# Performance work log

Hardware: AMD Instinct MI355X
Metric: run time of the kernel (lower is better)

The kernel has to match this reference:

```python
import jax, jax.numpy as jnp
import numpy as np
from jax import lax

EPS = 1e-6
BLOCK_SIZE = 64


def _feature_map(x, W):
    # x: (B,H,N,S,D), W: (H,D,F) -> (B,H,N,S,2F), computed in fp32
    u = jnp.einsum('bhnsd,hdf->bhnsf', x, W).astype(jnp.float32)
    return jnp.concatenate([jax.nn.softmax(u, axis=-1), jax.nn.softmax(-u, axis=-1)], axis=-1)


def setup_inputs() -> dict:
    key = jax.random.key(0)
    k1, k2, k3, k4, k5 = jax.random.split(key, 5)
    B, H, L, D, F = 2, 16, 4096, 64, 64
    q = jax.random.normal(k1, (B, H, L, D), dtype=jnp.float32)
    k = jax.random.normal(k2, (B, H, L, D), dtype=jnp.float32)
    v = jax.random.normal(k3, (B, H, L, D), dtype=jnp.float32)
    # hedgehog_weights initialized as eye(D,F) per head, perturbed so the test is non-trivial
    W = jnp.eye(D, F, dtype=jnp.float32)[None].repeat(H, axis=0) + 0.02 * jax.random.normal(k4, (H, D, F), dtype=jnp.float32)
    alpha = 0.1 * jax.random.normal(k5, (1, H, 1, 1), dtype=jnp.float32)
    return {"query_states": q, "key_states": k, "value_states": v,
            "hedgehog_weights": W, "alpha": alpha}


def _forward(q, k, v, W, alpha):
    B, H, L, D = q.shape
    S = BLOCK_SIZE
    N = L // S  # L chosen divisible by block size (no padding path)
    scaling = D ** (-0.5)
    F2 = 2 * W.shape[-1]

    qb = q.reshape(B, H, N, S, D)
    kb = k.reshape(B, H, N, S, D)
    vb = v.reshape(B, H, N, S, D)
    phi_q = _feature_map(qb, W)  # (B,H,N,S,2F) fp32
    phi_k = _feature_map(kb, W)
    w = jax.nn.sigmoid(alpha)    # (1,H,1,1)

    def step(carry, xs):
        S_state, Z_state = carry            # (B,H,2F,D), (B,H,2F)
        qn, kn, vn, pqn, pkn = xs           # per-block slices
        # linear-attention branch (pre-update state = clean history)
        lin_num = jnp.einsum('bhsf,bhfd->bhsd', pqn, S_state)
        lin_den = jnp.maximum(jnp.einsum('bhsf,bhf->bhs', pqn, Z_state)[..., None], EPS)
        # intra-block softmax branch (unnormalized, shared denominator)
        scores = jnp.einsum('bhsd,bhtd->bhst', qn, kn) * scaling
        a = jnp.exp(scores - scores.max(axis=-1, keepdims=True))
        sm_num = jnp.einsum('bhst,bhtd->bhsd', a, vn)
        sm_den = jnp.maximum(a.sum(axis=-1, keepdims=True), EPS)
        out = (w * sm_num + lin_num) / jnp.maximum(w * sm_den + lin_den, EPS)
        # state update with this block's keys/values
        S_state = S_state + jnp.einsum('bhsf,bhsd->bhfd', pkn, vn)
        Z_state = Z_state + pkn.sum(axis=-2)
        return (S_state, Z_state), out

    init = (jnp.zeros((B, H, F2, D), jnp.float32), jnp.zeros((B, H, F2), jnp.float32))
    xs = (jnp.moveaxis(qb, 2, 0), jnp.moveaxis(kb, 2, 0), jnp.moveaxis(vb, 2, 0),
          jnp.moveaxis(phi_q, 2, 0), jnp.moveaxis(phi_k, 2, 0))
    _, outs = lax.scan(step, init, xs)       # (N,B,H,S,D)
    return jnp.moveaxis(outs, 0, 2).reshape(B, H, L, D)


def reference(query_states, key_states, value_states, hedgehog_weights, alpha):
    return _forward(query_states, key_states, value_states, hedgehog_weights, alpha)
```

## Files before the change

### kernel.cpp

```cpp
#include <hip/hip_runtime.h>
#include <hip/hip_bf16.h>
#include <math.h>

constexpr int Bc = 2, Hc = 16, Lc = 4096, Dc = 64, Fc = 64;
constexpr int Sc = 64;
constexpr int Nc = Lc / Sc;
constexpr int F2 = 2 * Fc;
constexpr int BH = Bc * Hc;
constexpr int NBLK = BH * Nc;
constexpr float EPSf = 1e-6f;
constexpr float SCALE = 0.125f;

typedef short short8 __attribute__((ext_vector_type(8)));
typedef float f32x4 __attribute__((ext_vector_type(4)));
typedef unsigned short ushort;
typedef ushort ushort4v __attribute__((ext_vector_type(4)));

__device__ inline ushort f2bf(float x) {
    unsigned u = __builtin_bit_cast(unsigned, x);
    u = (u + 0x7fffu + ((u >> 16) & 1u)) >> 16;
    return (ushort)u;
}
__device__ inline float bf2f(ushort h) {
    return __builtin_bit_cast(float, ((unsigned)h) << 16);
}
__device__ inline f32x4 zero4() { f32x4 z = {0.f, 0.f, 0.f, 0.f}; return z; }

__device__ inline f32x4 mfma(short8 a, short8 b, f32x4 c) {
    return __builtin_amdgcn_mfma_f32_16x16x32_bf16(a, b, c, 0, 0, 0);
}

__device__ inline short8 ldfrag(const char* L, int row, int chunk, int rowbytes, int mask) {
    return *(const short8*)(L + row * rowbytes + ((chunk * 16) ^ ((row & mask) << 4)));
}

__device__ inline void stage_rm(const float* __restrict__ src, char* dst, int t) {
    #pragma unroll
    for (int i = 0; i < 4; ++i) {
        int e = t + i * 256;
        float4 x = ((const float4*)src)[e];
        int r = e >> 4;
        int c4 = (e & 15) * 4;
        ushort4v hv;
        hv[0] = f2bf(x.x); hv[1] = f2bf(x.y); hv[2] = f2bf(x.z); hv[3] = f2bf(x.w);
        *(ushort4v*)(dst + r * 128 + ((c4 * 2) ^ ((r & 7) << 4))) = hv;
    }
}

__device__ inline void stage_tr(const float* __restrict__ src, char* dst, int t) {
    int j = t & 63, g = t >> 6;
    #pragma unroll
    for (int i = 0; i < 4; ++i) {
        int i0 = g * 4 + i * 16;
        ushort4v hv;
        #pragma unroll
        for (int jj = 0; jj < 4; ++jj) hv[jj] = f2bf(src[(i0 + jj) * 64 + j]);
        *(ushort4v*)(dst + j * 128 + ((2 * i0) ^ ((j & 7) << 4))) = hv;
    }
}

__global__ __launch_bounds__(256) void passA(const float* __restrict__ K,
                                             const float* __restrict__ V,
                                             const float* __restrict__ W,
                                             ushort* __restrict__ wsS,
                                             float* __restrict__ wsZ)
{
    __shared__ __align__(16) char lds[40960];
    char* kR = lds;
    char* WT = lds + 8192;
    char* vT = lds + 16384;
    char* pT = lds + 24576;

    const int t = threadIdx.x, wv = t >> 6, l = t & 63, lr = l & 15, lg = l >> 4;
    const int bid = blockIdx.x, bh = bid >> 6, h = bh & (Hc - 1);
    const long base = (long)bh * Lc * Dc + (long)(bid & 63) * Sc * Dc;

    stage_rm(K + base, kR, t);
    stage_tr(W + (long)h * Dc * Fc, WT, t);
    stage_tr(V + base, vT, t);
    __syncthreads();

    short8 af0 = ldfrag(kR, 16 * wv + lr, lg, 128, 7);
    short8 af1 = ldfrag(kR, 16 * wv + lr, 4 + lg, 128, 7);
    f32x4 u0[4];
    #pragma unroll
    for (int tf = 0; tf < 4; ++tf) u0[tf] = zero4();
    #pragma unroll
    for (int tf = 0; tf < 4; ++tf) {
        u0[tf] = mfma(af0, ldfrag(WT, tf * 16 + lr, lg, 128, 7), u0[tf]);
        u0[tf] = mfma(af1, ldfrag(WT, tf * 16 + lr, 4 + lg, 128, 7), u0[tf]);
    }

    float pp[4][4], pn[4][4];
    #pragma unroll
    for (int r = 0; r < 4; ++r) {
        float mx = fmaxf(fmaxf(u0[0][r], u0[1][r]), fmaxf(u0[2][r], u0[3][r]));
        float mn = fminf(fminf(u0[0][r], u0[1][r]), fminf(u0[2][r], u0[3][r]));
        #pragma unroll
        for (int m = 1; m < 16; m <<= 1) {
            mx = fmaxf(mx, __shfl_xor(mx, m, 16));
            mn = fminf(mn, __shfl_xor(mn, m, 16));
        }
        float sp = 0.f, sn = 0.f;
        #pragma unroll
        for (int tf = 0; tf < 4; ++tf) {
            pp[tf][r] = __expf(u0[tf][r] - mx); sp += pp[tf][r];
            pn[tf][r] = __expf(mn - u0[tf][r]); sn += pn[tf][r];
        }
        #pragma unroll
        for (int m = 1; m < 16; m <<= 1) {
            sp += __shfl_xor(sp, m, 16);
            sn += __shfl_xor(sn, m, 16);
        }
        float rp = 1.f / sp, rn = 1.f / sn;
        #pragma unroll
        for (int tf = 0; tf < 4; ++tf) { pp[tf][r] *= rp; pn[tf][r] *= rn; }
    }

    #pragma unroll
    for (int tf = 0; tf < 4; ++tf)
        #pragma unroll
        for (int r = 0; r < 4; ++r) {
            int s = 16 * wv + lg * 4 + r;
            int f = tf * 16 + lr;
            *(ushort*)(pT + f * 128 + ((2 * s) ^ ((f & 7) << 4))) = f2bf(pp[tf][r]);
            int fn = 64 + f;
            *(ushort*)(pT + fn * 128 + ((2 * s) ^ ((fn & 7) << 4))) = f2bf(pn[tf][r]);
        }
    __syncthreads();

    short8 av0 = ldfrag(vT, 16 * wv + lr, lg, 128, 7);
    short8 av1 = ldfrag(vT, 16 * wv + lr, 4 + lg, 128, 7);
    f32x4 acc[8];
    #pragma unroll
    for (int tf = 0; tf < 8; ++tf) acc[tf] = zero4();
    #pragma unroll
    for (int tf = 0; tf < 8; ++tf) {
        acc[tf] = mfma(av0, ldfrag(pT, tf * 16 + lr, lg, 128, 7), acc[tf]);
        acc[tf] = mfma(av1, ldfrag(pT, tf * 16 + lr, 4 + lg, 128, 7), acc[tf]);
    }
    ushort* o = wsS + (long)bid * (F2 * Dc);
    #pragma unroll
    for (int tf = 0; tf < 8; ++tf)
        #pragma unroll
        for (int r = 0; r < 4; ++r) {
            int d = 16 * wv + lg * 4 + r;
            o[d * 128 + tf * 16 + lr] = f2bf(acc[tf][r]);
        }

    if (t < 128) {
        float z = 0.f;
        #pragma unroll
        for (int c = 0; c < 8; ++c) {
            short8 vv = ldfrag(pT, t, c, 128, 7);
            #pragma unroll
            for (int j = 0; j < 8; ++j) z += bf2f((ushort)vv[j]);
        }
        wsZ[(long)bid * F2 + t] = z;
    }
}

__global__ __launch_bounds__(256) void passB(ushort* __restrict__ wsS,
                                             float* __restrict__ wsZ)
{
    const int t = threadIdx.x;
    const int bh = blockIdx.x >> 3, chunk = blockIdx.x & 7;
    const int eoff = chunk * 1024 + t * 4;
    float c0 = 0.f, c1 = 0.f, c2 = 0.f, c3 = 0.f, zc = 0.f;
    const bool doZ = (chunk == 0) && (t < F2);
    for (int n = 0; n < Nc; ++n) {
        ushort4v* p = (ushort4v*)(wsS + (long)(bh * Nc + n) * 8192 + eoff);
        ushort4v x = *p;
        ushort4v cc;
        cc[0] = f2bf(c0); cc[1] = f2bf(c1); cc[2] = f2bf(c2); cc[3] = f2bf(c3);
        *p = cc;
        c0 += bf2f(x[0]); c1 += bf2f(x[1]); c2 += bf2f(x[2]); c3 += bf2f(x[3]);
        if (doZ) {
            float* pz = wsZ + (long)(bh * Nc + n) * F2 + t;
            float zv = *pz; *pz = zc; zc += zv;
        }
    }
}

__global__ __launch_bounds__(256) void passC(const float* __restrict__ Q,
                                             const float* __restrict__ K,
                                             const float* __restrict__ V,
                                             const float* __restrict__ W,
                                             const float* __restrict__ Alpha,
                                             const ushort* __restrict__ wsS,
                                             const float* __restrict__ wsZ,
                                             float* __restrict__ Out)
{
    __shared__ __align__(16) char lds[49664];
    char* qR   = lds;
    char* WT   = lds + 8192;
    char* kR   = lds + 16384;
    char* phiB = lds;
    char* aB   = lds + 16384;
    char* vT   = lds + 24576;
    char* St   = lds + 32768;
    float* sZ  = (float*)(lds + 49152);

    const int t = threadIdx.x, wv = t >> 6, l = t & 63, lr = l & 15, lg = l >> 4;
    const int bid = blockIdx.x, bh = bid >> 6, h = bh & (Hc - 1);
    const long base = (long)bh * Lc * Dc + (long)(bid & 63) * Sc * Dc;

    stage_rm(Q + base, qR, t);
    stage_tr(W + (long)h * Dc * Fc, WT, t);
    stage_rm(K + base, kR, t);
    stage_tr(V + base, vT, t);
    {
        const ushort* g = wsS + (long)bid * (F2 * Dc);
        #pragma unroll
        for (int i = 0; i < 4; ++i) {
            int c = t + i * 256;
            int d = c >> 4, fc = c & 15;
            short8 x = ((const short8*)g)[c];
            *(short8*)(St + d * 256 + ((fc * 16) ^ ((d & 15) << 4))) = x;
        }
        if (t < F2) sZ[t] = wsZ[(long)bid * F2 + t];
    }
    __syncthreads();

    short8 aq0 = ldfrag(qR, 16 * wv + lr, lg, 128, 7);
    short8 aq1 = ldfrag(qR, 16 * wv + lr, 4 + lg, 128, 7);
    f32x4 u0[4], s0[4];
    #pragma unroll
    for (int tf = 0; tf < 4; ++tf) { u0[tf] = zero4(); s0[tf] = zero4(); }
    #pragma unroll
    for (int tf = 0; tf < 4; ++tf) {
        u0[tf] = mfma(aq0, ldfrag(WT, tf * 16 + lr, lg, 128, 7), u0[tf]);
        u0[tf] = mfma(aq1, ldfrag(WT, tf * 16 + lr, 4 + lg, 128, 7), u0[tf]);
        s0[tf] = mfma(aq0, ldfrag(kR, tf * 16 + lr, lg, 128, 7), s0[tf]);
        s0[tf] = mfma(aq1, ldfrag(kR, tf * 16 + lr, 4 + lg, 128, 7), s0[tf]);
    }

    float pp[4][4], pn[4][4], sden[4], lden[4];
    #pragma unroll
    for (int r = 0; r < 4; ++r) {
        float mx = fmaxf(fmaxf(u0[0][r], u0[1][r]), fmaxf(u0[2][r], u0[3][r]));
        float mn = fminf(fminf(u0[0][r], u0[1][r]), fminf(u0[2][r], u0[3][r]));
        #pragma unroll
        for (int m = 1; m < 16; m <<= 1) {
            mx = fmaxf(mx, __shfl_xor(mx, m, 16));
            mn = fminf(mn, __shfl_xor(mn, m, 16));
        }
        float sp = 0.f, sn = 0.f;
        #pragma unroll
        for (int tf = 0; tf < 4; ++tf) {
            pp[tf][r] = __expf(u0[tf][r] - mx); sp += pp[tf][r];
            pn[tf][r] = __expf(mn - u0[tf][r]); sn += pn[tf][r];
        }
        #pragma unroll
        for (int m = 1; m < 16; m <<= 1) {
            sp += __shfl_xor(sp, m, 16);
            sn += __shfl_xor(sn, m, 16);
        }
        float rp = 1.f / sp, rn = 1.f / sn;
        float zd = 0.f;
        #pragma unroll
        for (int tf = 0; tf < 4; ++tf) {
            pp[tf][r] *= rp; pn[tf][r] *= rn;
            zd += pp[tf][r] * sZ[tf * 16 + lr] + pn[tf][r] * sZ[64 + tf * 16 + lr];
        }
        #pragma unroll
        for (int m = 1; m < 16; m <<= 1) zd += __shfl_xor(zd, m, 16);
        lden[r] = fmaxf(zd, EPSf);

        float sc[4];
        #pragma unroll
        for (int tf = 0; tf < 4; ++tf) sc[tf] = s0[tf][r] * SCALE;
        float m2 = fmaxf(fmaxf(sc[0], sc[1]), fmaxf(sc[2], sc[3]));
        #pragma unroll
        for (int m = 1; m < 16; m <<= 1) m2 = fmaxf(m2, __shfl_xor(m2, m, 16));
        float as = 0.f;
        #pragma unroll
        for (int tf = 0; tf < 4; ++tf) { sc[tf] = __expf(sc[tf] - m2); as += sc[tf]; }
        #pragma unroll
        for (int m = 1; m < 16; m <<= 1) as += __shfl_xor(as, m, 16);
        sden[r] = fmaxf(as, EPSf);
        #pragma unroll
        for (int tf = 0; tf < 4; ++tf) s0[tf][r] = sc[tf];
    }
    __syncthreads();

    #pragma unroll
    for (int tf = 0; tf < 4; ++tf)
        #pragma unroll
        for (int r = 0; r < 4; ++r) {
            int s = 16 * wv + lg * 4 + r;
            int f = tf * 16 + lr;
            *(ushort*)(phiB + s * 256 + ((2 * f) ^ ((s & 15) << 4))) = f2bf(pp[tf][r]);
            *(ushort*)(phiB + s * 256 + ((2 * (64 + f)) ^ ((s & 15) << 4))) = f2bf(pn[tf][r]);
            *(ushort*)(aB + s * 128 + ((2 * f) ^ ((s & 7) << 4))) = f2bf(s0[tf][r]);
        }
    __syncthreads();

    f32x4 acc[4];
    #pragma unroll
    for (int td = 0; td < 4; ++td) acc[td] = zero4();
    short8 aa0 = ldfrag(aB, 16 * wv + lr, lg, 128, 7);
    short8 aa1 = ldfrag(aB, 16 * wv + lr, 4 + lg, 128, 7);
    #pragma unroll
    for (int td = 0; td < 4; ++td) {
        acc[td] = mfma(aa0, ldfrag(vT, td * 16 + lr, lg, 128, 7), acc[td]);
        acc[td] = mfma(aa1, ldfrag(vT, td * 16 + lr, 4 + lg, 128, 7), acc[td]);
    }
    const float w = 1.f / (1.f + __expf(-Alpha[h]));
    #pragma unroll
    for (int td = 0; td < 4; ++td)
        #pragma unroll
        for (int r = 0; r < 4; ++r) acc[td][r] *= w;

    short8 pf[4];
    #pragma unroll
    for (int kc = 0; kc < 4; ++kc) pf[kc] = ldfrag(phiB, 16 * wv + lr, kc * 4 + lg, 256, 15);
    #pragma unroll
    for (int td = 0; td < 4; ++td)
        #pragma unroll
        for (int kc = 0; kc < 4; ++kc)
            acc[td] = mfma(pf[kc], ldfrag(St, td * 16 + lr, kc * 4 + lg, 256, 15), acc[td]);

    float* op = Out + base;
    #pragma unroll
    for (int r = 0; r < 4; ++r) {
        int s = 16 * wv + lg * 4 + r;
        float den = fmaxf(w * sden[r] + lden[r], EPSf);
        float inv = 1.f / den;
        #pragma unroll
        for (int td = 0; td < 4; ++td)
            op[s * 64 + td * 16 + lr] = acc[td][r] * inv;
    }
}

extern "C" void kernel_launch(void* const* d_in, const int* in_sizes, int n_in,
                              void* d_out, int out_size, void* d_ws, size_t ws_size,
                              hipStream_t stream)
{
    const float* q     = (const float*)d_in[0];
    const float* k     = (const float*)d_in[1];
    const float* v     = (const float*)d_in[2];
    const float* W     = (const float*)d_in[3];
    const float* alpha = (const float*)d_in[4];
    float* out = (float*)d_out;

    ushort* wsSb = (ushort*)d_ws;
    float*  wsZ  = (float*)((char*)d_ws + (size_t)NBLK * F2 * Dc * 2);

    passA<<<NBLK, 256, 0, stream>>>(k, v, W, wsSb, wsZ);
    passB<<<256, 256, 0, stream>>>(wsSb, wsZ);
    passC<<<NBLK, 256, 0, stream>>>(q, k, v, W, alpha, wsSb, wsZ, out);
}
```

Baseline: 86.84 us.

## Load MFMA fragments directly from global memory and batch scan loads

Adds a pre-pass that transposes W to bf16 once per head. passA and passC now read K, Q, W and the prefix state S directly from global memory into MFMA fragments instead of staging them in LDS, which shrinks LDS use and drops a barrier. passB issues 32 loads at a time per chunk before its serial prefix scan and moves the Z scan into separate blocks. The cost is more uncoalesced, redundant global reads: each K row is converted to bf16 several times in passC, and one extra kernel launch is added.

```diff
diff --git a/kernel.cpp b/kernel.cpp
--- a/kernel.cpp
+++ b/kernel.cpp
@@ -34,17 +34,16 @@
     return *(const short8*)(L + row * rowbytes + ((chunk * 16) ^ ((row & mask) << 4)));
 }
 
-__device__ inline void stage_rm(const float* __restrict__ src, char* dst, int t) {
-    #pragma unroll
-    for (int i = 0; i < 4; ++i) {
-        int e = t + i * 256;
-        float4 x = ((const float4*)src)[e];
-        int r = e >> 4;
-        int c4 = (e & 15) * 4;
-        ushort4v hv;
-        hv[0] = f2bf(x.x); hv[1] = f2bf(x.y); hv[2] = f2bf(x.z); hv[3] = f2bf(x.w);
-        *(ushort4v*)(dst + r * 128 + ((c4 * 2) ^ ((r & 7) << 4))) = hv;
-    }
+__device__ inline short8 gfrag_f32(const float* __restrict__ base, int row, int chunk) {
+    const float4* p = (const float4*)(base + row * 64 + chunk * 8);
+    float4 a = p[0], b = p[1];
+    short8 r;
+    r[0] = (short)f2bf(a.x); r[1] = (short)f2bf(a.y); r[2] = (short)f2bf(a.z); r[3] = (short)f2bf(a.w);
+    r[4] = (short)f2bf(b.x); r[5] = (short)f2bf(b.y); r[6] = (short)f2bf(b.z); r[7] = (short)f2bf(b.w);
+    return r;
+}
+__device__ inline short8 gfrag_bf16(const ushort* __restrict__ base, int row, int chunk, int rowlen) {
+    return *(const short8*)(base + row * rowlen + chunk * 8);
 }
 
 __device__ inline void stage_tr(const float* __restrict__ src, char* dst, int t) {
@@ -59,36 +58,48 @@
     }
 }
 
+__global__ __launch_bounds__(256) void passW(const float* __restrict__ W,
+                                             ushort* __restrict__ Wt)
+{
+    const int h = blockIdx.x, t = threadIdx.x;
+    const int f = t & 63, g = t >> 6;
+    const float* src = W + (long)h * 4096;
+    ushort* dst = Wt + (long)h * 4096;
+    #pragma unroll
+    for (int i = 0; i < 16; ++i) {
+        int d = g * 16 + i;
+        dst[f * 64 + d] = f2bf(src[d * 64 + f]);
+    }
+}
+
 __global__ __launch_bounds__(256) void passA(const float* __restrict__ K,
                                              const float* __restrict__ V,
-                                             const float* __restrict__ W,
+                                             const ushort* __restrict__ Wt,
                                              ushort* __restrict__ wsS,
                                              float* __restrict__ wsZ)
 {
-    __shared__ __align__(16) char lds[40960];
-    char* kR = lds;
-    char* WT = lds + 8192;
-    char* vT = lds + 16384;
-    char* pT = lds + 24576;
+    __shared__ __align__(16) char lds[24576];
+    char* vT = lds;
+    char* pT = lds + 8192;
 
     const int t = threadIdx.x, wv = t >> 6, l = t & 63, lr = l & 15, lg = l >> 4;
     const int bid = blockIdx.x, bh = bid >> 6, h = bh & (Hc - 1);
-    const long base = (long)bh * Lc * Dc + (long)(bid & 63) * Sc * Dc;
-
-    stage_rm(K + base, kR, t);
-    stage_tr(W + (long)h * Dc * Fc, WT, t);
+    const long base = (long)bh * (Lc * Dc) + (long)(bid & 63) * (Sc * Dc);
+
     stage_tr(V + base, vT, t);
-    __syncthreads();
-
-    short8 af0 = ldfrag(kR, 16 * wv + lr, lg, 128, 7);
-    short8 af1 = ldfrag(kR, 16 * wv + lr, 4 + lg, 128, 7);
+
+    const float* kp = K + base;
+    const ushort* wt = Wt + (long)h * 4096;
+
+    short8 ak0 = gfrag_f32(kp, 16 * wv + lr, lg);
+    short8 ak1 = gfrag_f32(kp, 16 * wv + lr, 4 + lg);
     f32x4 u0[4];
     #pragma unroll
     for (int tf = 0; tf < 4; ++tf) u0[tf] = zero4();
     #pragma unroll
     for (int tf = 0; tf < 4; ++tf) {
-        u0[tf] = mfma(af0, ldfrag(WT, tf * 16 + lr, lg, 128, 7), u0[tf]);
-        u0[tf] = mfma(af1, ldfrag(WT, tf * 16 + lr, 4 + lg, 128, 7), u0[tf]);
+        u0[tf] = mfma(ak0, gfrag_bf16(wt, tf * 16 + lr, lg, 64), u0[tf]);
+        u0[tf] = mfma(ak1, gfrag_bf16(wt, tf * 16 + lr, 4 + lg, 64), u0[tf]);
     }
 
     float pp[4][4], pn[4][4];
@@ -164,20 +175,37 @@
                                              float* __restrict__ wsZ)
 {
     const int t = threadIdx.x;
+    if (blockIdx.x >= 256) {
+        const int bh = blockIdx.x - 256;
+        if (t < 128) {
+            float zc = 0.f, zb[32];
+            #pragma unroll
+            for (int h2 = 0; h2 < 2; ++h2) {
+                float* zp = wsZ + ((long)bh * 64 + h2 * 32) * 128 + t;
+                #pragma unroll
+                for (int i = 0; i < 32; ++i) zb[i] = zp[i * 128];
+                #pragma unroll
+                for (int i = 0; i < 32; ++i) { float x = zb[i]; zp[i * 128] = zc; zc += x; }
+            }
+        }
+        return;
+    }
     const int bh = blockIdx.x >> 3, chunk = blockIdx.x & 7;
-    const int eoff = chunk * 1024 + t * 4;
-    float c0 = 0.f, c1 = 0.f, c2 = 0.f, c3 = 0.f, zc = 0.f;
-    const bool doZ = (chunk == 0) && (t < F2);
-    for (int n = 0; n < Nc; ++n) {
-        ushort4v* p = (ushort4v*)(wsS + (long)(bh * Nc + n) * 8192 + eoff);
-        ushort4v x = *p;
-        ushort4v cc;
-        cc[0] = f2bf(c0); cc[1] = f2bf(c1); cc[2] = f2bf(c2); cc[3] = f2bf(c3);
-        *p = cc;
-        c0 += bf2f(x[0]); c1 += bf2f(x[1]); c2 += bf2f(x[2]); c3 += bf2f(x[3]);
-        if (doZ) {
-            float* pz = wsZ + (long)(bh * Nc + n) * F2 + t;
-            float zv = *pz; *pz = zc; zc += zv;
+    ushort* p = wsS + (long)bh * 64 * 8192 + chunk * 1024 + t * 4;
+    float c0 = 0.f, c1 = 0.f, c2 = 0.f, c3 = 0.f;
+    ushort4v buf[32];
+    #pragma unroll
+    for (int h2 = 0; h2 < 2; ++h2) {
+        ushort4v* pp = (ushort4v*)(p + (long)h2 * 32 * 8192);
+        #pragma unroll
+        for (int i = 0; i < 32; ++i) buf[i] = pp[i * 2048];
+        #pragma unroll
+        for (int i = 0; i < 32; ++i) {
+            ushort4v x = buf[i];
+            ushort4v cc;
+            cc[0] = f2bf(c0); cc[1] = f2bf(c1); cc[2] = f2bf(c2); cc[3] = f2bf(c3);
+            pp[i * 2048] = cc;
+            c0 += bf2f(x[0]); c1 += bf2f(x[1]); c2 += bf2f(x[2]); c3 += bf2f(x[3]);
         }
     }
 }
@@ -185,54 +213,44 @@
 __global__ __launch_bounds__(256) void passC(const float* __restrict__ Q,
                                              const float* __restrict__ K,
                                              const float* __restrict__ V,
-                                             const float* __restrict__ W,
+                                             const ushort* __restrict__ Wt,
                                              const float* __restrict__ Alpha,
                                              const ushort* __restrict__ wsS,
                                              const float* __restrict__ wsZ,
                                              float* __restrict__ Out)
 {
-    __shared__ __align__(16) char lds[49664];
-    char* qR   = lds;
-    char* WT   = lds + 8192;
-    char* kR   = lds + 16384;
-    char* phiB = lds;
-    char* aB   = lds + 16384;
-    char* vT   = lds + 24576;
-    char* St   = lds + 32768;
-    float* sZ  = (float*)(lds + 49152);
-
+    __shared__ __align__(16) char lds[32768];
+    char* vT = lds;
     const int t = threadIdx.x, wv = t >> 6, l = t & 63, lr = l & 15, lg = l >> 4;
+    char* phiL = lds + 8192 + wv * 4096;
+    char* aL   = lds + 24576 + wv * 2048;
+
     const int bid = blockIdx.x, bh = bid >> 6, h = bh & (Hc - 1);
-    const long base = (long)bh * Lc * Dc + (long)(bid & 63) * Sc * Dc;
-
-    stage_rm(Q + base, qR, t);
-    stage_tr(W + (long)h * Dc * Fc, WT, t);
-    stage_rm(K + base, kR, t);
+    const long base = (long)bh * (Lc * Dc) + (long)(bid & 63) * (Sc * Dc);
+
     stage_tr(V + base, vT, t);
-    {
-        const ushort* g = wsS + (long)bid * (F2 * Dc);
-        #pragma unroll
-        for (int i = 0; i < 4; ++i) {
-            int c = t + i * 256;
-            int d = c >> 4, fc = c & 15;
-            short8 x = ((const short8*)g)[c];
-            *(short8*)(St + d * 256 + ((fc * 16) ^ ((d & 15) << 4))) = x;
-        }
-        if (t < F2) sZ[t] = wsZ[(long)bid * F2 + t];
-    }
-    __syncthreads();
-
-    short8 aq0 = ldfrag(qR, 16 * wv + lr, lg, 128, 7);
-    short8 aq1 = ldfrag(qR, 16 * wv + lr, 4 + lg, 128, 7);
+
+    const float* qp = Q + base;
+    const float* kp = K + base;
+    const ushort* wt = Wt + (long)h * 4096;
+    const float* zp = wsZ + (long)bid * F2;
+
+    float zv[4], zn[4];
+    #pragma unroll
+    for (int tf = 0; tf < 4; ++tf) { zv[tf] = zp[tf * 16 + lr]; zn[tf] = zp[64 + tf * 16 + lr]; }
+    const float w = 1.f / (1.f + __expf(-Alpha[h]));
+
+    short8 aq0 = gfrag_f32(qp, 16 * wv + lr, lg);
+    short8 aq1 = gfrag_f32(qp, 16 * wv + lr, 4 + lg);
     f32x4 u0[4], s0[4];
     #pragma unroll
     for (int tf = 0; tf < 4; ++tf) { u0[tf] = zero4(); s0[tf] = zero4(); }
     #pragma unroll
     for (int tf = 0; tf < 4; ++tf) {
-        u0[tf] = mfma(aq0, ldfrag(WT, tf * 16 + lr, lg, 128, 7), u0[tf]);
-        u0[tf] = mfma(aq1, ldfrag(WT, tf * 16 + lr, 4 + lg, 128, 7), u0[tf]);
-        s0[tf] = mfma(aq0, ldfrag(kR, tf * 16 + lr, lg, 128, 7), s0[tf]);
-        s0[tf] = mfma(aq1, ldfrag(kR, tf * 16 + lr, 4 + lg, 128, 7), s0[tf]);
+        u0[tf] = mfma(aq0, gfrag_bf16(wt, tf * 16 + lr, lg, 64), u0[tf]);
+        u0[tf] = mfma(aq1, gfrag_bf16(wt, tf * 16 + lr, 4 + lg, 64), u0[tf]);
+        s0[tf] = mfma(aq0, gfrag_f32(kp, tf * 16 + lr, lg), s0[tf]);
+        s0[tf] = mfma(aq1, gfrag_f32(kp, tf * 16 + lr, 4 + lg), s0[tf]);
     }
 
     float pp[4][4], pn[4][4], sden[4], lden[4];
@@ -261,7 +279,7 @@
         #pragma unroll
         for (int tf = 0; tf < 4; ++tf) {
             pp[tf][r] *= rp; pn[tf][r] *= rn;
-            zd += pp[tf][r] * sZ[tf * 16 + lr] + pn[tf][r] * sZ[64 + tf * 16 + lr];
+            zd += pp[tf][r] * zv[tf] + pn[tf][r] * zn[tf];
         }
         #pragma unroll
         for (int m = 1; m < 16; m <<= 1) zd += __shfl_xor(zd, m, 16);
@@ -282,31 +300,31 @@
         #pragma unroll
         for (int tf = 0; tf < 4; ++tf) s0[tf][r] = sc[tf];
     }
+
+    #pragma unroll
+    for (int tf = 0; tf < 4; ++tf)
+        #pragma unroll
+        for (int r = 0; r < 4; ++r) {
+            int sl = lg * 4 + r;
+            int f = tf * 16 + lr;
+            *(ushort*)(phiL + sl * 256 + ((2 * f) ^ ((sl & 15) << 4))) = f2bf(pp[tf][r]);
+            *(ushort*)(phiL + sl * 256 + ((2 * (64 + f)) ^ ((sl & 15) << 4))) = f2bf(pn[tf][r]);
+            *(ushort*)(aL + sl * 128 + ((2 * f) ^ ((sl & 7) << 4))) = f2bf(s0[tf][r]);
+        }
+
     __syncthreads();
 
-    #pragma unroll
-    for (int tf = 0; tf < 4; ++tf)
-        #pragma unroll
-        for (int r = 0; r < 4; ++r) {
-            int s = 16 * wv + lg * 4 + r;
-            int f = tf * 16 + lr;
-            *(ushort*)(phiB + s * 256 + ((2 * f) ^ ((s & 15) << 4))) = f2bf(pp[tf][r]);
-            *(ushort*)(phiB + s * 256 + ((2 * (64 + f)) ^ ((s & 15) << 4))) = f2bf(pn[tf][r]);
-            *(ushort*)(aB + s * 128 + ((2 * f) ^ ((s & 7) << 4))) = f2bf(s0[tf][r]);
-        }
-    __syncthreads();
-
+    const ushort* Sg = wsS + (long)bid * (F2 * Dc);
     f32x4 acc[4];
     #pragma unroll
     for (int td = 0; td < 4; ++td) acc[td] = zero4();
-    short8 aa0 = ldfrag(aB, 16 * wv + lr, lg, 128, 7);
-    short8 aa1 = ldfrag(aB, 16 * wv + lr, 4 + lg, 128, 7);
+    short8 aa0 = ldfrag(aL, lr, lg, 128, 7);
+    short8 aa1 = ldfrag(aL, lr, 4 + lg, 128, 7);
     #pragma unroll
     for (int td = 0; td < 4; ++td) {
         acc[td] = mfma(aa0, ldfrag(vT, td * 16 + lr, lg, 128, 7), acc[td]);
         acc[td] = mfma(aa1, ldfrag(vT, td * 16 + lr, 4 + lg, 128, 7), acc[td]);
     }
-    const float w = 1.f / (1.f + __expf(-Alpha[h]));
     #pragma unroll
     for (int td = 0; td < 4; ++td)
         #pragma unroll
@@ -314,12 +332,12 @@
 
     short8 pf[4];
     #pragma unroll
-    for (int kc = 0; kc < 4; ++kc) pf[kc] = ldfrag(phiB, 16 * wv + lr, kc * 4 + lg, 256, 15);
+    for (int kc = 0; kc < 4; ++kc) pf[kc] = ldfrag(phiL, lr, kc * 4 + lg, 256, 15);
     #pragma unroll
     for (int td = 0; td < 4; ++td)
         #pragma unroll
         for (int kc = 0; kc < 4; ++kc)
-            acc[td] = mfma(pf[kc], ldfrag(St, td * 16 + lr, kc * 4 + lg, 256, 15), acc[td]);
+            acc[td] = mfma(pf[kc], gfrag_bf16(Sg, td * 16 + lr, kc * 4 + lg, 128), acc[td]);
 
     float* op = Out + base;
     #pragma unroll
@@ -346,8 +364,10 @@
 
     ushort* wsSb = (ushort*)d_ws;
     float*  wsZ  = (float*)((char*)d_ws + (size_t)NBLK * F2 * Dc * 2);
-
-    passA<<<NBLK, 256, 0, stream>>>(k, v, W, wsSb, wsZ);
-    passB<<<256, 256, 0, stream>>>(wsSb, wsZ);
-    passC<<<NBLK, 256, 0, stream>>>(q, k, v, W, alpha, wsSb, wsZ, out);
-}
+    ushort* Wtb  = (ushort*)((char*)wsZ + (size_t)NBLK * F2 * 4);
+
+    passW<<<Hc, 256, 0, stream>>>(W, Wtb);
+    passA<<<NBLK, 256, 0, stream>>>(k, v, Wtb, wsSb, wsZ);
+    passB<<<288, 256, 0, stream>>>(wsSb, wsZ);
+    passC<<<NBLK, 256, 0, stream>>>(q, k, v, Wtb, alpha, wsSb, wsZ, out);
+}
```

After: 94.75 us. 9.1% more time.

## Process chunks of four blocks per workgroup with in-register running state

Applied to the files above, without the earlier changes.

Each workgroup now handles a chunk of four 64-row blocks instead of one. The first pass accumulates the chunk's key-value state in fp32, the scan pass works over 16 chunks per head instead of 64 blocks, and the final pass carries the state in registers while it updates block by block. This shrinks the workspace traffic and the length of the serial scan, and it drops the bf16 rounding of prefix states. In exchange the final pass runs a sequential four-step loop per workgroup with fewer workgroups (512), uses more LDS (about 74 KB), and drops the max-subtraction in the feature-map softmax, which could overflow for large inputs.

```diff
diff --git a/kernel.cpp b/kernel.cpp
--- a/kernel.cpp
+++ b/kernel.cpp
@@ -2,12 +2,13 @@
 #include <hip/hip_bf16.h>
 #include <math.h>
 
-constexpr int Bc = 2, Hc = 16, Lc = 4096, Dc = 64, Fc = 64;
-constexpr int Sc = 64;
+constexpr int Hc = 16, Lc = 4096, Dc = 64, Sc = 64;
 constexpr int Nc = Lc / Sc;
-constexpr int F2 = 2 * Fc;
-constexpr int BH = Bc * Hc;
-constexpr int NBLK = BH * Nc;
+constexpr int F2 = 128;
+constexpr int BH = 32;
+constexpr int CH = 4;
+constexpr int CPB = Nc / CH;
+constexpr int NCHUNK = BH * CPB;
 constexpr float EPSf = 1e-6f;
 constexpr float SCALE = 0.125f;
 
@@ -21,9 +22,6 @@
     u = (u + 0x7fffu + ((u >> 16) & 1u)) >> 16;
     return (ushort)u;
 }
-__device__ inline float bf2f(ushort h) {
-    return __builtin_bit_cast(float, ((unsigned)h) << 16);
-}
 __device__ inline f32x4 zero4() { f32x4 z = {0.f, 0.f, 0.f, 0.f}; return z; }
 
 __device__ inline f32x4 mfma(short8 a, short8 b, f32x4 c) {
@@ -32,6 +30,15 @@
 
 __device__ inline short8 ldfrag(const char* L, int row, int chunk, int rowbytes, int mask) {
     return *(const short8*)(L + row * rowbytes + ((chunk * 16) ^ ((row & mask) << 4)));
+}
+
+__device__ inline short8 gfrag_f32(const float* __restrict__ base, int row, int chunk) {
+    const float4* p = (const float4*)(base + row * 64 + chunk * 8);
+    float4 a = p[0], b = p[1];
+    short8 r;
+    r[0] = (short)f2bf(a.x); r[1] = (short)f2bf(a.y); r[2] = (short)f2bf(a.z); r[3] = (short)f2bf(a.w);
+    r[4] = (short)f2bf(b.x); r[5] = (short)f2bf(b.y); r[6] = (short)f2bf(b.z); r[7] = (short)f2bf(b.w);
+    return r;
 }
 
 __device__ inline void stage_rm(const float* __restrict__ src, char* dst, int t) {
@@ -59,277 +66,360 @@
     }
 }
 
-__global__ __launch_bounds__(256) void passA(const float* __restrict__ K,
-                                             const float* __restrict__ V,
-                                             const float* __restrict__ W,
-                                             ushort* __restrict__ wsS,
-                                             float* __restrict__ wsZ)
+__global__ __launch_bounds__(256) void passF1(const float* __restrict__ K,
+                                              const float* __restrict__ V,
+                                              const float* __restrict__ W,
+                                              float* __restrict__ wsC,
+                                              float* __restrict__ wsZc)
 {
-    __shared__ __align__(16) char lds[40960];
-    char* kR = lds;
-    char* WT = lds + 8192;
-    char* vT = lds + 16384;
-    char* pT = lds + 24576;
+    __shared__ __align__(16) char lds[51200];
+    char* kR  = lds;
+    char* vT0 = lds + 8192;
+    char* vT1 = lds + 16384;
+    char* WTl = lds + 24576;
+    char* pT  = lds + 32768;
+    float* Zp = (float*)(lds + 49152);
 
     const int t = threadIdx.x, wv = t >> 6, l = t & 63, lr = l & 15, lg = l >> 4;
-    const int bid = blockIdx.x, bh = bid >> 6, h = bh & (Hc - 1);
-    const long base = (long)bh * Lc * Dc + (long)(bid & 63) * Sc * Dc;
-
-    stage_rm(K + base, kR, t);
-    stage_tr(W + (long)h * Dc * Fc, WT, t);
-    stage_tr(V + base, vT, t);
+    const int bid = blockIdx.x, bh = bid >> 4, c = bid & (CPB - 1), h = bh & (Hc - 1);
+    const long hbase = (long)bh * (Lc * Dc);
+
+    stage_tr(W + (long)h * (Dc * 64), WTl, t);
+
+    f32x4 acc[8];
+    #pragma unroll
+    for (int i = 0; i < 8; ++i) acc[i] = zero4();
+    float zpa[4] = {0.f,0.f,0.f,0.f}, zna[4] = {0.f,0.f,0.f,0.f};
+
+    for (int tt = 0; tt < CH; ++tt) {
+        char* vT = (tt & 1) ? vT1 : vT0;
+        const long base = hbase + (long)(c * CH + tt) * (Sc * Dc);
+        stage_rm(K + base, kR, t);
+        stage_tr(V + base, vT, t);
+        __syncthreads();
+
+        short8 ak0 = ldfrag(kR, 16*wv + lr, lg, 128, 7);
+        short8 ak1 = ldfrag(kR, 16*wv + lr, 4 + lg, 128, 7);
+        f32x4 u0[4];
+        #pragma unroll
+        for (int tf = 0; tf < 4; ++tf) u0[tf] = zero4();
+        #pragma unroll
+        for (int tf = 0; tf < 4; ++tf) {
+            u0[tf] = mfma(ak0, ldfrag(WTl, tf*16 + lr, lg, 128, 7), u0[tf]);
+            u0[tf] = mfma(ak1, ldfrag(WTl, tf*16 + lr, 4 + lg, 128, 7), u0[tf]);
+        }
+        float pp[4][4], pn[4][4];
+        #pragma unroll
+        for (int r = 0; r < 4; ++r) {
+            float sp = 0.f, sn = 0.f;
+            #pragma unroll
+            for (int tf = 0; tf < 4; ++tf) {
+                pp[tf][r] = __expf(u0[tf][r]);  sp += pp[tf][r];
+                pn[tf][r] = __expf(-u0[tf][r]); sn += pn[tf][r];
+            }
+            #pragma unroll
+            for (int m = 1; m < 16; m <<= 1) { sp += __shfl_xor(sp, m, 16); sn += __shfl_xor(sn, m, 16); }
+            float rp = 1.f / sp, rn = 1.f / sn;
+            #pragma unroll
+            for (int tf = 0; tf < 4; ++tf) {
+                pp[tf][r] *= rp; pn[tf][r] *= rn;
+                zpa[tf] += pp[tf][r]; zna[tf] += pn[tf][r];
+            }
+        }
+        #pragma unroll
+        for (int tf = 0; tf < 4; ++tf)
+            #pragma unroll
+            for (int r = 0; r < 4; ++r) {
+                int s = 16*wv + lg*4 + r;
+                int f = tf*16 + lr;
+                *(ushort*)(pT + f*128 + ((2*s) ^ ((f & 7) << 4))) = f2bf(pp[tf][r]);
+                int fn = 64 + f;
+                *(ushort*)(pT + fn*128 + ((2*s) ^ ((fn & 7) << 4))) = f2bf(pn[tf][r]);
+            }
+        __syncthreads();
+
+        short8 av0 = ldfrag(vT, 16*wv + lr, lg, 128, 7);
+        short8 av1 = ldfrag(vT, 16*wv + lr, 4 + lg, 128, 7);
+        #pragma unroll
+        for (int tf = 0; tf < 8; ++tf) {
+            acc[tf] = mfma(av0, ldfrag(pT, tf*16 + lr, lg, 128, 7), acc[tf]);
+            acc[tf] = mfma(av1, ldfrag(pT, tf*16 + lr, 4 + lg, 128, 7), acc[tf]);
+        }
+    }
+
+    float* oc = wsC + (long)bid * 8192;
+    #pragma unroll
+    for (int tf = 0; tf < 8; ++tf)
+        #pragma unroll
+        for (int r = 0; r < 4; ++r)
+            oc[(16*wv + lg*4 + r) * 128 + tf*16 + lr] = acc[tf][r];
+
+    #pragma unroll
+    for (int tf = 0; tf < 4; ++tf) {
+        zpa[tf] += __shfl_xor(zpa[tf], 16); zpa[tf] += __shfl_xor(zpa[tf], 32);
+        zna[tf] += __shfl_xor(zna[tf], 16); zna[tf] += __shfl_xor(zna[tf], 32);
+    }
+    if (l < 16) {
+        #pragma unroll
+        for (int tf = 0; tf < 4; ++tf) {
+            Zp[wv*128 + tf*16 + lr]      = zpa[tf];
+            Zp[wv*128 + 64 + tf*16 + lr] = zna[tf];
+        }
+    }
     __syncthreads();
-
-    short8 af0 = ldfrag(kR, 16 * wv + lr, lg, 128, 7);
-    short8 af1 = ldfrag(kR, 16 * wv + lr, 4 + lg, 128, 7);
-    f32x4 u0[4];
-    #pragma unroll
-    for (int tf = 0; tf < 4; ++tf) u0[tf] = zero4();
-    #pragma unroll
-    for (int tf = 0; tf < 4; ++tf) {
-        u0[tf] = mfma(af0, ldfrag(WT, tf * 16 + lr, lg, 128, 7), u0[tf]);
-        u0[tf] = mfma(af1, ldfrag(WT, tf * 16 + lr, 4 + lg, 128, 7), u0[tf]);
-    }
-
-    float pp[4][4], pn[4][4];
-    #pragma unroll
-    for (int r = 0; r < 4; ++r) {
-        float mx = fmaxf(fmaxf(u0[0][r], u0[1][r]), fmaxf(u0[2][r], u0[3][r]));
-        float mn = fminf(fminf(u0[0][r], u0[1][r]), fminf(u0[2][r], u0[3][r]));
-        #pragma unroll
-        for (int m = 1; m < 16; m <<= 1) {
-            mx = fmaxf(mx, __shfl_xor(mx, m, 16));
-            mn = fminf(mn, __shfl_xor(mn, m, 16));
-        }
-        float sp = 0.f, sn = 0.f;
-        #pragma unroll
-        for (int tf = 0; tf < 4; ++tf) {
-            pp[tf][r] = __expf(u0[tf][r] - mx); sp += pp[tf][r];
-            pn[tf][r] = __expf(mn - u0[tf][r]); sn += pn[tf][r];
-        }
-        #pragma unroll
-        for (int m = 1; m < 16; m <<= 1) {
-            sp += __shfl_xor(sp, m, 16);
-            sn += __shfl_xor(sn, m, 16);
-        }
-        float rp = 1.f / sp, rn = 1.f / sn;
-        #pragma unroll
-        for (int tf = 0; tf < 4; ++tf) { pp[tf][r] *= rp; pn[tf][r] *= rn; }
-    }
-
-    #pragma unroll
-    for (int tf = 0; tf < 4; ++tf)
-        #pragma unroll
-        for (int r = 0; r < 4; ++r) {
-            int s = 16 * wv + lg * 4 + r;
-            int f = tf * 16 + lr;
-            *(ushort*)(pT + f * 128 + ((2 * s) ^ ((f & 7) << 4))) = f2bf(pp[tf][r]);
-            int fn = 64 + f;
-            *(ushort*)(pT + fn * 128 + ((2 * s) ^ ((fn & 7) << 4))) = f2bf(pn[tf][r]);
-        }
-    __syncthreads();
-
-    short8 av0 = ldfrag(vT, 16 * wv + lr, lg, 128, 7);
-    short8 av1 = ldfrag(vT, 16 * wv + lr, 4 + lg, 128, 7);
-    f32x4 acc[8];
-    #pragma unroll
-    for (int tf = 0; tf < 8; ++tf) acc[tf] = zero4();
-    #pragma unroll
-    for (int tf = 0; tf < 8; ++tf) {
-        acc[tf] = mfma(av0, ldfrag(pT, tf * 16 + lr, lg, 128, 7), acc[tf]);
-        acc[tf] = mfma(av1, ldfrag(pT, tf * 16 + lr, 4 + lg, 128, 7), acc[tf]);
-    }
-    ushort* o = wsS + (long)bid * (F2 * Dc);
-    #pragma unroll
-    for (int tf = 0; tf < 8; ++tf)
-        #pragma unroll
-        for (int r = 0; r < 4; ++r) {
-            int d = 16 * wv + lg * 4 + r;
-            o[d * 128 + tf * 16 + lr] = f2bf(acc[tf][r]);
-        }
-
-    if (t < 128) {
-        float z = 0.f;
-        #pragma unroll
-        for (int c = 0; c < 8; ++c) {
-            short8 vv = ldfrag(pT, t, c, 128, 7);
-            #pragma unroll
-            for (int j = 0; j < 8; ++j) z += bf2f((ushort)vv[j]);
-        }
-        wsZ[(long)bid * F2 + t] = z;
-    }
-}
-
-__global__ __launch_bounds__(256) void passB(ushort* __restrict__ wsS,
-                                             float* __restrict__ wsZ)
+    if (t < 128)
+        wsZc[(long)bid * 128 + t] = Zp[t] + Zp[128 + t] + Zp[256 + t] + Zp[384 + t];
+}
+
+__global__ __launch_bounds__(256) void passF2(float* __restrict__ wsC,
+                                              float* __restrict__ wsZc)
 {
     const int t = threadIdx.x;
-    const int bh = blockIdx.x >> 3, chunk = blockIdx.x & 7;
-    const int eoff = chunk * 1024 + t * 4;
-    float c0 = 0.f, c1 = 0.f, c2 = 0.f, c3 = 0.f, zc = 0.f;
-    const bool doZ = (chunk == 0) && (t < F2);
-    for (int n = 0; n < Nc; ++n) {
-        ushort4v* p = (ushort4v*)(wsS + (long)(bh * Nc + n) * 8192 + eoff);
-        ushort4v x = *p;
-        ushort4v cc;
-        cc[0] = f2bf(c0); cc[1] = f2bf(c1); cc[2] = f2bf(c2); cc[3] = f2bf(c3);
-        *p = cc;
-        c0 += bf2f(x[0]); c1 += bf2f(x[1]); c2 += bf2f(x[2]); c3 += bf2f(x[3]);
-        if (doZ) {
-            float* pz = wsZ + (long)(bh * Nc + n) * F2 + t;
-            float zv = *pz; *pz = zc; zc += zv;
-        }
-    }
-}
-
-__global__ __launch_bounds__(256) void passC(const float* __restrict__ Q,
-                                             const float* __restrict__ K,
-                                             const float* __restrict__ V,
-                                             const float* __restrict__ W,
-                                             const float* __restrict__ Alpha,
-                                             const ushort* __restrict__ wsS,
-                                             const float* __restrict__ wsZ,
-                                             float* __restrict__ Out)
+    if (blockIdx.x >= 256) {
+        const int bh = blockIdx.x - 256;
+        if (t < 128) {
+            float* zp = wsZc + (long)bh * CPB * 128 + t;
+            float buf[CPB];
+            #pragma unroll
+            for (int i = 0; i < CPB; ++i) buf[i] = zp[(long)i * 128];
+            float cz = 0.f;
+            #pragma unroll
+            for (int i = 0; i < CPB; ++i) { float x = buf[i]; zp[(long)i * 128] = cz; cz += x; }
+        }
+        return;
+    }
+    const int bh = blockIdx.x >> 3, part = blockIdx.x & 7;
+    float* p = wsC + (long)bh * CPB * 8192 + part * 1024 + t * 4;
+    float4 buf[CPB];
+    #pragma unroll
+    for (int i = 0; i < CPB; ++i) buf[i] = *(const float4*)(p + (long)i * 8192);
+    float4 cr = make_float4(0.f, 0.f, 0.f, 0.f);
+    #pragma unroll
+    for (int i = 0; i < CPB; ++i) {
+        float4 x = buf[i];
+        *(float4*)(p + (long)i * 8192) = cr;
+        cr.x += x.x; cr.y += x.y; cr.z += x.z; cr.w += x.w;
+    }
+}
+
+__global__ __launch_bounds__(256) void passF3(const float* __restrict__ Q,
+                                              const float* __restrict__ K,
+                                              const float* __restrict__ V,
+                                              const float* __restrict__ W,
+                                              const float* __restrict__ Alpha,
+                                              const float* __restrict__ wsC,
+                                              const float* __restrict__ wsZc,
+                                              float* __restrict__ Out)
 {
-    __shared__ __align__(16) char lds[49664];
-    char* qR   = lds;
-    char* WT   = lds + 8192;
-    char* kR   = lds + 16384;
-    char* phiB = lds;
-    char* aB   = lds + 16384;
-    char* vT   = lds + 24576;
-    char* St   = lds + 32768;
-    float* sZ  = (float*)(lds + 49152);
+    __shared__ __align__(16) char lds[75776];
+    char* kR   = lds;
+    char* vT0  = lds + 8192;
+    char* vT1  = lds + 16384;
+    char* WTl  = lds + 24576;
+    char* Stb  = lds + 32768;
+    char* phiP = lds + 49152;
+    char* aLb  = lds + 65536;
+    float* Zp  = (float*)(lds + 73728);
 
     const int t = threadIdx.x, wv = t >> 6, l = t & 63, lr = l & 15, lg = l >> 4;
-    const int bid = blockIdx.x, bh = bid >> 6, h = bh & (Hc - 1);
-    const long base = (long)bh * Lc * Dc + (long)(bid & 63) * Sc * Dc;
-
-    stage_rm(Q + base, qR, t);
-    stage_tr(W + (long)h * Dc * Fc, WT, t);
-    stage_rm(K + base, kR, t);
-    stage_tr(V + base, vT, t);
+    char* phiL = phiP + wv * 4096;
+    char* aL   = aLb + wv * 2048;
+    char* pT   = phiP;
+
+    const int bid = blockIdx.x, bh = bid >> 4, c = bid & (CPB - 1), h = bh & (Hc - 1);
+    const long hbase = (long)bh * (Lc * Dc);
+
+    stage_tr(W + (long)h * (Dc * 64), WTl, t);
+
+    f32x4 sacc[8];
     {
-        const ushort* g = wsS + (long)bid * (F2 * Dc);
-        #pragma unroll
-        for (int i = 0; i < 4; ++i) {
-            int c = t + i * 256;
-            int d = c >> 4, fc = c & 15;
-            short8 x = ((const short8*)g)[c];
-            *(short8*)(St + d * 256 + ((fc * 16) ^ ((d & 15) << 4))) = x;
-        }
-        if (t < F2) sZ[t] = wsZ[(long)bid * F2 + t];
-    }
-    __syncthreads();
-
-    short8 aq0 = ldfrag(qR, 16 * wv + lr, lg, 128, 7);
-    short8 aq1 = ldfrag(qR, 16 * wv + lr, 4 + lg, 128, 7);
-    f32x4 u0[4], s0[4];
-    #pragma unroll
-    for (int tf = 0; tf < 4; ++tf) { u0[tf] = zero4(); s0[tf] = zero4(); }
-    #pragma unroll
-    for (int tf = 0; tf < 4; ++tf) {
-        u0[tf] = mfma(aq0, ldfrag(WT, tf * 16 + lr, lg, 128, 7), u0[tf]);
-        u0[tf] = mfma(aq1, ldfrag(WT, tf * 16 + lr, 4 + lg, 128, 7), u0[tf]);
-        s0[tf] = mfma(aq0, ldfrag(kR, tf * 16 + lr, lg, 128, 7), s0[tf]);
-        s0[tf] = mfma(aq1, ldfrag(kR, tf * 16 + lr, 4 + lg, 128, 7), s0[tf]);
-    }
-
-    float pp[4][4], pn[4][4], sden[4], lden[4];
-    #pragma unroll
-    for (int r = 0; r < 4; ++r) {
-        float mx = fmaxf(fmaxf(u0[0][r], u0[1][r]), fmaxf(u0[2][r], u0[3][r]));
-        float mn = fminf(fminf(u0[0][r], u0[1][r]), fminf(u0[2][r], u0[3][r]));
-        #pragma unroll
-        for (int m = 1; m < 16; m <<= 1) {
-            mx = fmaxf(mx, __shfl_xor(mx, m, 16));
-            mn = fminf(mn, __shfl_xor(mn, m, 16));
-        }
-        float sp = 0.f, sn = 0.f;
+        const float* s0p = wsC + (long)bid * 8192;
+        #pragma unroll
+        for (int tf = 0; tf < 8; ++tf)
+            #pragma unroll
+            for (int r = 0; r < 4; ++r)
+                sacc[tf][r] = s0p[(16*wv + lg*4 + r) * 128 + tf*16 + lr];
+    }
+    float zv[4], zn_[4];
+    {
+        const float* z0 = wsZc + (long)bid * 128;
+        #pragma unroll
+        for (int tf = 0; tf < 4; ++tf) { zv[tf] = z0[tf*16 + lr]; zn_[tf] = z0[64 + tf*16 + lr]; }
+    }
+    const float w = 1.f / (1.f + __expf(-Alpha[h]));
+
+    for (int tt = 0; tt < CH; ++tt) {
+        char* vT = (tt & 1) ? vT1 : vT0;
+        const long base = hbase + (long)(c * CH + tt) * (Sc * Dc);
+
+        #pragma unroll
+        for (int tf = 0; tf < 8; ++tf)
+            #pragma unroll
+            for (int r = 0; r < 4; ++r) {
+                int d = 16*wv + lg*4 + r;
+                int f = tf*16 + lr;
+                *(ushort*)(Stb + d*256 + ((2*f) ^ ((d & 15) << 4))) = f2bf(sacc[tf][r]);
+            }
+        stage_rm(K + base, kR, t);
+        stage_tr(V + base, vT, t);
+        short8 aq0 = gfrag_f32(Q + base, 16*wv + lr, lg);
+        short8 aq1 = gfrag_f32(Q + base, 16*wv + lr, 4 + lg);
+        __syncthreads();
+
+        short8 ak0 = ldfrag(kR, 16*wv + lr, lg, 128, 7);
+        short8 ak1 = ldfrag(kR, 16*wv + lr, 4 + lg, 128, 7);
+        f32x4 uq[4], uk[4], sc0[4];
+        #pragma unroll
+        for (int tf = 0; tf < 4; ++tf) { uq[tf] = zero4(); uk[tf] = zero4(); sc0[tf] = zero4(); }
+        const bool upd = (tt != CH - 1);
         #pragma unroll
         for (int tf = 0; tf < 4; ++tf) {
-            pp[tf][r] = __expf(u0[tf][r] - mx); sp += pp[tf][r];
-            pn[tf][r] = __expf(mn - u0[tf][r]); sn += pn[tf][r];
-        }
-        #pragma unroll
-        for (int m = 1; m < 16; m <<= 1) {
-            sp += __shfl_xor(sp, m, 16);
-            sn += __shfl_xor(sn, m, 16);
-        }
-        float rp = 1.f / sp, rn = 1.f / sn;
-        float zd = 0.f;
-        #pragma unroll
-        for (int tf = 0; tf < 4; ++tf) {
-            pp[tf][r] *= rp; pn[tf][r] *= rn;
-            zd += pp[tf][r] * sZ[tf * 16 + lr] + pn[tf][r] * sZ[64 + tf * 16 + lr];
-        }
-        #pragma unroll
-        for (int m = 1; m < 16; m <<= 1) zd += __shfl_xor(zd, m, 16);
-        lden[r] = fmaxf(zd, EPSf);
-
-        float sc[4];
-        #pragma unroll
-        for (int tf = 0; tf < 4; ++tf) sc[tf] = s0[tf][r] * SCALE;
-        float m2 = fmaxf(fmaxf(sc[0], sc[1]), fmaxf(sc[2], sc[3]));
-        #pragma unroll
-        for (int m = 1; m < 16; m <<= 1) m2 = fmaxf(m2, __shfl_xor(m2, m, 16));
-        float as = 0.f;
-        #pragma unroll
-        for (int tf = 0; tf < 4; ++tf) { sc[tf] = __expf(sc[tf] - m2); as += sc[tf]; }
-        #pragma unroll
-        for (int m = 1; m < 16; m <<= 1) as += __shfl_xor(as, m, 16);
-        sden[r] = fmaxf(as, EPSf);
-        #pragma unroll
-        for (int tf = 0; tf < 4; ++tf) s0[tf][r] = sc[tf];
-    }
-    __syncthreads();
-
-    #pragma unroll
-    for (int tf = 0; tf < 4; ++tf)
+            short8 bw0 = ldfrag(WTl, tf*16 + lr, lg, 128, 7);
+            short8 bw1 = ldfrag(WTl, tf*16 + lr, 4 + lg, 128, 7);
+            uq[tf] = mfma(aq0, bw0, uq[tf]); uq[tf] = mfma(aq1, bw1, uq[tf]);
+            sc0[tf] = mfma(aq0, ldfrag(kR, tf*16 + lr, lg, 128, 7), sc0[tf]);
+            sc0[tf] = mfma(aq1, ldfrag(kR, tf*16 + lr, 4 + lg, 128, 7), sc0[tf]);
+            if (upd) { uk[tf] = mfma(ak0, bw0, uk[tf]); uk[tf] = mfma(ak1, bw1, uk[tf]); }
+        }
+
+        float lden[4], sden[4];
         #pragma unroll
         for (int r = 0; r < 4; ++r) {
-            int s = 16 * wv + lg * 4 + r;
-            int f = tf * 16 + lr;
-            *(ushort*)(phiB + s * 256 + ((2 * f) ^ ((s & 15) << 4))) = f2bf(pp[tf][r]);
-            *(ushort*)(phiB + s * 256 + ((2 * (64 + f)) ^ ((s & 15) << 4))) = f2bf(pn[tf][r]);
-            *(ushort*)(aB + s * 128 + ((2 * f) ^ ((s & 7) << 4))) = f2bf(s0[tf][r]);
-        }
-    __syncthreads();
-
-    f32x4 acc[4];
-    #pragma unroll
-    for (int td = 0; td < 4; ++td) acc[td] = zero4();
-    short8 aa0 = ldfrag(aB, 16 * wv + lr, lg, 128, 7);
-    short8 aa1 = ldfrag(aB, 16 * wv + lr, 4 + lg, 128, 7);
-    #pragma unroll
-    for (int td = 0; td < 4; ++td) {
-        acc[td] = mfma(aa0, ldfrag(vT, td * 16 + lr, lg, 128, 7), acc[td]);
-        acc[td] = mfma(aa1, ldfrag(vT, td * 16 + lr, 4 + lg, 128, 7), acc[td]);
-    }
-    const float w = 1.f / (1.f + __expf(-Alpha[h]));
-    #pragma unroll
-    for (int td = 0; td < 4; ++td)
-        #pragma unroll
-        for (int r = 0; r < 4; ++r) acc[td][r] *= w;
-
-    short8 pf[4];
-    #pragma unroll
-    for (int kc = 0; kc < 4; ++kc) pf[kc] = ldfrag(phiB, 16 * wv + lr, kc * 4 + lg, 256, 15);
-    #pragma unroll
-    for (int td = 0; td < 4; ++td)
-        #pragma unroll
-        for (int kc = 0; kc < 4; ++kc)
-            acc[td] = mfma(pf[kc], ldfrag(St, td * 16 + lr, kc * 4 + lg, 256, 15), acc[td]);
-
-    float* op = Out + base;
-    #pragma unroll
-    for (int r = 0; r < 4; ++r) {
-        int s = 16 * wv + lg * 4 + r;
-        float den = fmaxf(w * sden[r] + lden[r], EPSf);
-        float inv = 1.f / den;
+            float pqp[4], pqn[4];
+            float sp = 0.f, sn = 0.f;
+            #pragma unroll
+            for (int tf = 0; tf < 4; ++tf) {
+                pqp[tf] = __expf(uq[tf][r]);  sp += pqp[tf];
+                pqn[tf] = __expf(-uq[tf][r]); sn += pqn[tf];
+            }
+            #pragma unroll
+            for (int m = 1; m < 16; m <<= 1) { sp += __shfl_xor(sp, m, 16); sn += __shfl_xor(sn, m, 16); }
+            float rp = 1.f / sp, rn = 1.f / sn;
+            float zd = 0.f;
+            #pragma unroll
+            for (int tf = 0; tf < 4; ++tf) {
+                pqp[tf] *= rp; pqn[tf] *= rn;
+                zd += pqp[tf] * zv[tf] + pqn[tf] * zn_[tf];
+            }
+            #pragma unroll
+            for (int m = 1; m < 16; m <<= 1) zd += __shfl_xor(zd, m, 16);
+            lden[r] = fmaxf(zd, EPSf);
+            int sl = lg*4 + r;
+            #pragma unroll
+            for (int tf = 0; tf < 4; ++tf) {
+                int f = tf*16 + lr;
+                *(ushort*)(phiL + sl*256 + ((2*f) ^ ((sl & 15) << 4))) = f2bf(pqp[tf]);
+                *(ushort*)(phiL + sl*256 + ((2*(64 + f)) ^ ((sl & 15) << 4))) = f2bf(pqn[tf]);
+            }
+        }
+
+        #pragma unroll
+        for (int r = 0; r < 4; ++r) {
+            float s[4];
+            #pragma unroll
+            for (int tf = 0; tf < 4; ++tf) s[tf] = sc0[tf][r] * SCALE;
+            float m2 = fmaxf(fmaxf(s[0], s[1]), fmaxf(s[2], s[3]));
+            #pragma unroll
+            for (int m = 1; m < 16; m <<= 1) m2 = fmaxf(m2, __shfl_xor(m2, m, 16));
+            float as = 0.f;
+            #pragma unroll
+            for (int tf = 0; tf < 4; ++tf) { s[tf] = __expf(s[tf] - m2); as += s[tf]; }
+            #pragma unroll
+            for (int m = 1; m < 16; m <<= 1) as += __shfl_xor(as, m, 16);
+            sden[r] = fmaxf(as, EPSf);
+            int sl = lg*4 + r;
+            #pragma unroll
+            for (int tf = 0; tf < 4; ++tf)
+                *(ushort*)(aL + sl*128 + ((2*(tf*16 + lr)) ^ ((sl & 7) << 4))) = f2bf(w * s[tf]);
+        }
+
+        f32x4 oacc[4];
+        #pragma unroll
+        for (int td = 0; td < 4; ++td) oacc[td] = zero4();
+        short8 aa0 = ldfrag(aL, lr, lg, 128, 7);
+        short8 aa1 = ldfrag(aL, lr, 4 + lg, 128, 7);
+        #pragma unroll
+        for (int td = 0; td < 4; ++td) {
+            oacc[td] = mfma(aa0, ldfrag(vT, td*16 + lr, lg, 128, 7), oacc[td]);
+            oacc[td] = mfma(aa1, ldfrag(vT, td*16 + lr, 4 + lg, 128, 7), oacc[td]);
+        }
+        short8 pf[4];
+        #pragma unroll
+        for (int kc = 0; kc < 4; ++kc) pf[kc] = ldfrag(phiL, lr, kc*4 + lg, 256, 15);
         #pragma unroll
         for (int td = 0; td < 4; ++td)
-            op[s * 64 + td * 16 + lr] = acc[td][r] * inv;
+            #pragma unroll
+            for (int kc = 0; kc < 4; ++kc)
+                oacc[td] = mfma(pf[kc], ldfrag(Stb, td*16 + lr, kc*4 + lg, 256, 15), oacc[td]);
+
+        float* op = Out + base;
+        #pragma unroll
+        for (int r = 0; r < 4; ++r) {
+            int s = 16*wv + lg*4 + r;
+            float inv = 1.f / fmaxf(w * sden[r] + lden[r], EPSf);
+            #pragma unroll
+            for (int td = 0; td < 4; ++td)
+                op[s*64 + td*16 + lr] = oacc[td][r] * inv;
+        }
+
+        if (upd) {
+            __syncthreads();
+            float pkp[4][4], pkn[4][4];
+            float zr[4] = {0.f,0.f,0.f,0.f}, zrn[4] = {0.f,0.f,0.f,0.f};
+            #pragma unroll
+            for (int r = 0; r < 4; ++r) {
+                float sp = 0.f, sn = 0.f;
+                #pragma unroll
+                for (int tf = 0; tf < 4; ++tf) {
+                    pkp[tf][r] = __expf(uk[tf][r]);  sp += pkp[tf][r];
+                    pkn[tf][r] = __expf(-uk[tf][r]); sn += pkn[tf][r];
+                }
+                #pragma unroll
+                for (int m = 1; m < 16; m <<= 1) { sp += __shfl_xor(sp, m, 16); sn += __shfl_xor(sn, m, 16); }
+                float rp = 1.f / sp, rn = 1.f / sn;
+                #pragma unroll
+                for (int tf = 0; tf < 4; ++tf) {
+                    pkp[tf][r] *= rp; pkn[tf][r] *= rn;
+                    zr[tf] += pkp[tf][r]; zrn[tf] += pkn[tf][r];
+                }
+            }
+            #pragma unroll
+            for (int tf = 0; tf < 4; ++tf)
+                #pragma unroll
+                for (int r = 0; r < 4; ++r) {
+                    int s = 16*wv + lg*4 + r;
+                    int f = tf*16 + lr;
+                    *(ushort*)(pT + f*128 + ((2*s) ^ ((f & 7) << 4))) = f2bf(pkp[tf][r]);
+                    int fn = 64 + f;
+                    *(ushort*)(pT + fn*128 + ((2*s) ^ ((fn & 7) << 4))) = f2bf(pkn[tf][r]);
+                }
+            #pragma unroll
+            for (int tf = 0; tf < 4; ++tf) {
+                zr[tf] += __shfl_xor(zr[tf], 16);  zr[tf] += __shfl_xor(zr[tf], 32);
+                zrn[tf] += __shfl_xor(zrn[tf], 16); zrn[tf] += __shfl_xor(zrn[tf], 32);
+            }
+            if (l < 16) {
+                #pragma unroll
+                for (int tf = 0; tf < 4; ++tf) {
+                    Zp[wv*128 + tf*16 + lr]      = zr[tf];
+                    Zp[wv*128 + 64 + tf*16 + lr] = zrn[tf];
+                }
+            }
+            __syncthreads();
+            short8 av0 = ldfrag(vT, 16*wv + lr, lg, 128, 7);
+            short8 av1 = ldfrag(vT, 16*wv + lr, 4 + lg, 128, 7);
+            #pragma unroll
+            for (int tf = 0; tf < 8; ++tf) {
+                sacc[tf] = mfma(av0, ldfrag(pT, tf*16 + lr, lg, 128, 7), sacc[tf]);
+                sacc[tf] = mfma(av1, ldfrag(pT, tf*16 + lr, 4 + lg, 128, 7), sacc[tf]);
+            }
+            #pragma unroll
+            for (int tf = 0; tf < 4; ++tf) {
+                int f = tf*16 + lr;
+                zv[tf]  += Zp[f] + Zp[128 + f] + Zp[256 + f] + Zp[384 + f];
+                zn_[tf] += Zp[64 + f] + Zp[192 + f] + Zp[320 + f] + Zp[448 + f];
+            }
+        }
     }
 }
 
@@ -344,10 +434,10 @@
     const float* alpha = (const float*)d_in[4];
     float* out = (float*)d_out;
 
-    ushort* wsSb = (ushort*)d_ws;
-    float*  wsZ  = (float*)((char*)d_ws + (size_t)NBLK * F2 * Dc * 2);
-
-    passA<<<NBLK, 256, 0, stream>>>(k, v, W, wsSb, wsZ);
-    passB<<<256, 256, 0, stream>>>(wsSb, wsZ);
-    passC<<<NBLK, 256, 0, stream>>>(q, k, v, W, alpha, wsSb, wsZ, out);
-}
+    float* wsC  = (float*)d_ws;
+    float* wsZc = wsC + (size_t)NCHUNK * 8192;
+
+    passF1<<<NCHUNK, 256, 0, stream>>>(k, v, W, wsC, wsZc);
+    passF2<<<288, 256, 0, stream>>>(wsC, wsZc);
+    passF3<<<NCHUNK, 256, 0, stream>>>(q, k, v, W, alpha, wsC, wsZc, out);
+}
```

New measurement: 104.6 us. 20.5% more time.
